# Performance work log

Hardware: AMD Instinct MI355X
Metric: run time of the kernel (lower is better)

The kernel has to match this reference:

```python
import jax, jax.numpy as jnp
import numpy as np

N, E = 50000, 800000
F_IN, F_OUT, H = 128, 16, 8
NEG_SLOPE = 0.2  # PyG GATConv default
EPS = 1e-5       # LayerNorm eps


def setup_inputs() -> dict:
    key = jax.random.key(0)
    ks = jax.random.split(key, 8)
    x = jax.random.normal(ks[0], (N, F_IN), dtype=jnp.float32)
    edge_index = jax.random.randint(ks[1], (2, E), 0, N, dtype=jnp.int32)
    s_in = 1.0 / np.sqrt(F_IN)
    s_f = 1.0 / np.sqrt(F_OUT)
    W = jax.random.normal(ks[2], (F_IN, H * F_OUT), dtype=jnp.float32) * s_in
    att_src = jax.random.normal(ks[3], (H, F_OUT), dtype=jnp.float32) * s_f
    att_dst = jax.random.normal(ks[4], (H, F_OUT), dtype=jnp.float32) * s_f
    bias = jnp.zeros((H * F_OUT,), dtype=jnp.float32)
    gamma = jnp.ones((H * F_OUT,), dtype=jnp.float32)
    beta = jnp.zeros((H * F_OUT,), dtype=jnp.float32)
    return {"x": x, "edge_index": edge_index, "W": W, "att_src": att_src,
            "att_dst": att_dst, "bias": bias, "gamma": gamma, "beta": beta}


def _gat_layer(x, edge_index, W, att_src, att_dst, bias, gamma, beta):
    n = x.shape[0]
    # add self loops (PyG GATConv default add_self_loops=True)
    loop = jnp.arange(n, dtype=edge_index.dtype)
    src = jnp.concatenate([edge_index[0], loop])  # message source j
    dst = jnp.concatenate([edge_index[1], loop])  # message target i

    xp = (x @ W).reshape(n, H, F_OUT)                      # [N,H,F]
    a_src = jnp.einsum('nhf,hf->nh', xp, att_src)          # [N,H]
    a_dst = jnp.einsum('nhf,hf->nh', xp, att_dst)          # [N,H]

    e = a_src[src] + a_dst[dst]                            # [E+N,H]
    e = jax.nn.leaky_relu(e, NEG_SLOPE)
    # softmax over incoming edges per destination node
    m = jax.ops.segment_max(e, dst, num_segments=n)        # [N,H]
    e = jnp.exp(e - m[dst])
    z = jax.ops.segment_sum(e, dst, num_segments=n)        # [N,H]
    alpha = e / jnp.where(z[dst] > 0, z[dst], 1.0)         # [E+N,H]

    msg = alpha[:, :, None] * xp[src]                      # [E+N,H,F]
    out = jax.ops.segment_sum(msg, dst, num_segments=n)    # [N,H,F]
    out = out.reshape(n, H * F_OUT) + bias

    # LayerNorm over feature dim
    mu = out.mean(axis=-1, keepdims=True)
    var = out.var(axis=-1, keepdims=True)
    return (out - mu) * jax.lax.rsqrt(var + EPS) * gamma + beta


def reference(x, edge_index, W, att_src, att_dst, bias, gamma, beta):
    return _gat_layer(x, edge_index, W, att_src, att_dst, bias, gamma, beta)
```

## Files before the change

kernel.cpp:

```cpp
#include <hip/hip_runtime.h>
#include <math.h>

#define F_IN 128
#define NHD 8
#define FEAT 128
#define NEG_SLOPE 0.2f
#define LN_EPS 1e-5f
#define BSH 7
#define BMSK 127
#define NPQ 16
#define CAP 48
#define EPB 2048
#define NBMAX 512
#define BCAP 6144
#define WCOLS 144

typedef __bf16 v8bf __attribute__((ext_vector_type(8)));
typedef __bf16 v2bf __attribute__((ext_vector_type(2)));
typedef float f32x4 __attribute__((ext_vector_type(4)));

__global__ __launch_bounds__(256) void k_wt(const float* __restrict__ W,
                                            const float* __restrict__ att_src,
                                            const float* __restrict__ att_dst,
                                            __bf16* __restrict__ WT,
                                            int* __restrict__ gcnt, int NB) {
    int idx = blockIdx.x * 256 + threadIdx.x;
    if (idx < NB) gcnt[idx] = 0;
    int c = idx >> 7, k = idx & 127;
    float v;
    if (c < 128) {
        v = W[k * 128 + c];
    } else if (c < 136) {
        int h = c - 128;
        float s = 0.f;
#pragma unroll
        for (int f = 0; f < 16; ++f) s += W[k * 128 + h * 16 + f] * att_src[h * 16 + f];
        v = s;
    } else {
        int h = c - 136;
        float s = 0.f;
#pragma unroll
        for (int f = 0; f < 16; ++f) s += W[k * 128 + h * 16 + f] * att_dst[h * 16 + f];
        v = s;
    }
    WT[c * 128 + k] = (__bf16)v;
}

__global__ __launch_bounds__(512) void k_fused(const float* __restrict__ x,
                                               const __bf16* __restrict__ WT,
                                               __bf16* __restrict__ xp16,
                                               float* __restrict__ a_src,
                                               float* __restrict__ a_dst,
                                               const int* __restrict__ src,
                                               const int* __restrict__ dst,
                                               unsigned int* __restrict__ sorted2,
                                               int* __restrict__ gcnt,
                                               int n, int E, int Ga) {
    __shared__ __align__(16) char smem[34816];
    if ((int)blockIdx.x < Ga) {
        unsigned int* sorted_l = (unsigned int*)smem;
        int* lcnt = (int*)(smem + 8192);
        int* loff = (int*)(smem + 8192 + 2048);
        int* wtot = (int*)(smem + 8192 + 2048 + 2052);
        int* wexcl = (int*)(smem + 8192 + 2048 + 2052 + 32);
        int* goff = (int*)(smem + 8192 + 2048 + 2052 + 64);
        int NB = (n + BMSK) >> BSH;
        int tid = threadIdx.x, lane = tid & 63, wid = tid >> 6;
        long base0 = (long)blockIdx.x * EPB;
        long total = (long)E + n;
        if (tid < NB) lcnt[tid] = 0;
        __syncthreads();

        int s0[4], d0[4];
        bool val[4];
        long e0 = base0 + (long)tid * 4;
        if (e0 + 3 < E) {
            int4 sv = *(const int4*)(src + e0);
            int4 dv = *(const int4*)(dst + e0);
            s0[0] = sv.x; s0[1] = sv.y; s0[2] = sv.z; s0[3] = sv.w;
            d0[0] = dv.x; d0[1] = dv.y; d0[2] = dv.z; d0[3] = dv.w;
            val[0] = val[1] = val[2] = val[3] = true;
        } else {
#pragma unroll
            for (int j = 0; j < 4; ++j) {
                long e = e0 + j;
                val[j] = (e < total);
                s0[j] = d0[j] = 0;
                if (val[j]) {
                    if (e < E) { s0[j] = src[e]; d0[j] = dst[e]; }
                    else { s0[j] = d0[j] = (int)(e - E); }
                }
            }
        }
#pragma unroll
        for (int j = 0; j < 4; ++j)
            if (val[j]) atomicAdd(&lcnt[d0[j] >> BSH], 1);
        __syncthreads();

        int v = (tid < NB) ? lcnt[tid] : 0;
        int xx = v;
#pragma unroll
        for (int o = 1; o < 64; o <<= 1) {
            int t2 = __shfl_up(xx, o);
            if (lane >= o) xx += t2;
        }
        if (lane == 63) wtot[wid] = xx;
        __syncthreads();
        if (wid == 0 && lane < 8) {
            int s = wtot[lane];
            int y = s;
#pragma unroll
            for (int o = 1; o < 8; o <<= 1) {
                int t2 = __shfl_up(y, o);
                if (lane >= o) y += t2;
            }
            wexcl[lane] = y - s;
        }
        __syncthreads();
        int excl = wexcl[wid] + xx - v;
        if (tid < NB) loff[tid] = excl;
        if (tid == NB - 1) loff[NB] = excl + v;
        __syncthreads();
        if (tid < NB) lcnt[tid] = loff[tid];
        __syncthreads();
#pragma unroll
        for (int j = 0; j < 4; ++j) {
            if (val[j]) {
                int b = d0[j] >> BSH;
                int pos = atomicAdd(&lcnt[b], 1);
                sorted_l[pos] = ((unsigned)b << 23) | ((unsigned)s0[j] << 7) |
                                (unsigned)(d0[j] & BMSK);
            }
        }
        __syncthreads();
        if (tid < NB) {
            int len = loff[tid + 1] - loff[tid];
            goff[tid] = (len > 0) ? atomicAdd(&gcnt[tid], len) : 0;
        }
        __syncthreads();
        int tv = loff[NB];
        for (int i = tid; i < tv; i += 512) {
            unsigned int u = sorted_l[i];
            int b = (int)(u >> 23);
            int r = goff[b] + (i - loff[b]);
            if (r < BCAP)
                sorted2[(long)b * BCAP + r] = u & 0x7FFFFFu;
        }
    } else {
        __bf16 (*xs)[136] = (__bf16 (*)[136])smem;
        __bf16 (*ot)[136] = (__bf16 (*)[136])(smem + 17408);
        int gb = blockIdx.x - Ga;
        int tid = threadIdx.x;
        int rowbase = gb * 64;
        {
            int i4 = tid;
#pragma unroll
            for (int rep = 0; rep < 4; ++rep, i4 += 512) {
                int r = i4 >> 5, c4 = i4 & 31;
                int gr = rowbase + r; if (gr > n - 1) gr = n - 1;
                float4 xv = *(const float4*)(x + (long)gr * 128 + c4 * 4);
                __bf16* p = &xs[r][c4 * 4];
                p[0] = (__bf16)xv.x; p[1] = (__bf16)xv.y;
                p[2] = (__bf16)xv.z; p[3] = (__bf16)xv.w;
            }
        }
        __syncthreads();
        int wv = tid >> 6;
        int lane = tid & 63;
        int m = lane & 15, quad = lane >> 4;
        int colbase = wv * 16;
        const __bf16* wcol = WT + (colbase + m) * 128;
        v8bf wf[4];
#pragma unroll
        for (int kk = 0; kk < 4; ++kk)
            wf[kk] = *(const v8bf*)(wcol + kk * 32 + quad * 8);
        v8bf wf2[4];
        if (wv < 4) {
            const __bf16* wcol2 = WT + (128 + m) * 128;
#pragma unroll
            for (int kk = 0; kk < 4; ++kk)
                wf2[kk] = *(const v8bf*)(wcol2 + kk * 32 + quad * 8);
        }
#pragma unroll
        for (int t = 0; t < 4; ++t) {
            int rb = t * 16;
            f32x4 acc = {0.f, 0.f, 0.f, 0.f};
#pragma unroll
            for (int kk = 0; kk < 4; ++kk) {
                v8bf a = *(const v8bf*)(&xs[rb + m][kk * 32 + quad * 8]);
                acc = __builtin_amdgcn_mfma_f32_16x16x32_bf16(a, wf[kk], acc, 0, 0, 0);
            }
#pragma unroll
            for (int r = 0; r < 4; ++r)
                ot[rb + quad * 4 + r][colbase + m] = (__bf16)acc[r];
        }
        if (wv < 4) {
            int rb = wv * 16;
            f32x4 acc = {0.f, 0.f, 0.f, 0.f};
#pragma unroll
            for (int kk = 0; kk < 4; ++kk) {
                v8bf a = *(const v8bf*)(&xs[rb + m][kk * 32 + quad * 8]);
                acc = __builtin_amdgcn_mfma_f32_16x16x32_bf16(a, wf2[kk], acc, 0, 0, 0);
            }
#pragma unroll
            for (int r = 0; r < 4; ++r) {
                int row = rowbase + rb + quad * 4 + r;
                if (row < n) {
                    if (m < 8) a_src[row * 8 + m] = acc[r];
                    else       a_dst[row * 8 + (m - 8)] = acc[r];
                }
            }
        }
        __syncthreads();
        int r0 = tid >> 4, c8 = tid & 15;
#pragma unroll
        for (int pass = 0; pass < 2; ++pass) {
            int r = r0 + pass * 32;
            int gr = rowbase + r;
            if (gr < n) {
                v8bf vv = *(const v8bf*)(&ot[r][c8 * 8]);
                *(v8bf*)(xp16 + (long)gr * FEAT + c8 * 8) = vv;
            }
        }
    }
}

__global__ __launch_bounds__(256) void k_ba(const unsigned int* __restrict__ sorted2,
                                            const int* __restrict__ bcnt,
                                            const float* __restrict__ a_src,
                                            const float* __restrict__ a_dst,
                                            const __bf16* __restrict__ xp16,
                                            const float* __restrict__ bias,
                                            const float* __restrict__ gamma,
                                            const float* __restrict__ beta,
                                            const int* __restrict__ src,
                                            const int* __restrict__ dst,
                                            float* __restrict__ out, int n, int E) {
    __shared__ int slds[NPQ * CAP];
    __shared__ int lc[NPQ];
    __shared__ float adst_s[NPQ * NHD];
    int b = blockIdx.x >> 3;
    int q = blockIdx.x & 7;
    int tid = threadIdx.x;
    int node0 = (b << BSH) + q * NPQ;
    if (tid < NPQ) lc[tid] = 0;
    if (tid < NPQ * NHD) {
        int nd = node0 + (tid >> 3);
        adst_s[tid] = (nd < n) ? a_dst[nd * NHD + (tid & 7)] : 0.f;
    }
    __syncthreads();

    int cnt_b = bcnt[b]; if (cnt_b > BCAP) cnt_b = BCAP;
    const unsigned int* sg = sorted2 + (long)b * BCAP;
    int qlo = q * NPQ;
    for (int i = tid; i < cnt_b; i += 256) {
        unsigned int u = sg[i];
        int dl = (int)(u & BMSK) - qlo;
        if ((unsigned)dl < (unsigned)NPQ) {
            int p = atomicAdd(&lc[dl], 1);
            if (p < CAP) slds[dl * CAP + p] = (int)(u >> BSH);
        }
    }
    __syncthreads();
    if (tid < NPQ) {
        int cc = lc[tid]; if (cc > CAP) cc = CAP;
        int pad = (cc + 7) & ~7; if (pad > CAP) pad = CAP;
        for (int p = cc; p < pad; ++p) slds[tid * CAP + p] = 0;
    }
    __syncthreads();

    int lane = tid & 63, wv = tid >> 6;
    int h = lane & 7, j8 = lane >> 3;
    float2 bs = *(const float2*)(bias + 2 * lane);
    float2 g  = *(const float2*)(gamma + 2 * lane);
    float2 bt = *(const float2*)(beta + 2 * lane);

    for (int i = wv; i < NPQ; i += 4) {
        int node = node0 + i;
        if (node >= n) break;
        int cnt = lc[i];
        float acc0 = 0.f, acc1 = 0.f, inv;

        if (cnt <= CAP) {
            const int* row = slds + i * CAP;
            float b_h = adst_s[i * NHD + h];
            float zacc = 0.f;
            for (int base = 0; base < cnt; base += 8) {
                int s_my = row[base + j8];
                float e = a_src[s_my * NHD + h] + b_h;
                e = e > 0.f ? e : NEG_SLOPE * e;
                float w_my = (base + j8 < cnt) ? __expf(e) : 0.f;
                zacc += w_my;
                int ss[8];
#pragma unroll
                for (int j = 0; j < 8; ++j) ss[j] = row[base + j];
                float2 vals[8];
#pragma unroll
                for (int j = 0; j < 8; ++j) {
                    v2bf p = *(const v2bf*)(xp16 + (long)ss[j] * FEAT + 2 * lane);
                    vals[j] = make_float2((float)p[0], (float)p[1]);
                }
#pragma unroll
                for (int j = 0; j < 8; ++j) {
                    float w = __shfl(w_my, j * 8 + j8);
                    acc0 = fmaf(w, vals[j].x, acc0);
                    acc1 = fmaf(w, vals[j].y, acc1);
                }
            }
            zacc += __shfl_xor(zacc, 8);
            zacc += __shfl_xor(zacc, 16);
            zacc += __shfl_xor(zacc, 32);
            float z = __shfl(zacc, j8);
            inv = 1.f / z;
        } else {
            float b_h = a_dst[node * NHD + j8];
            float z = 0.f;
            {
                float e = a_src[node * NHD + j8] + b_h;
                e = e > 0.f ? e : NEG_SLOPE * e;
                float w = __expf(e);
                z += w;
                v2bf p = *(const v2bf*)(xp16 + (long)node * FEAT + 2 * lane);
                acc0 = fmaf(w, (float)p[0], acc0);
                acc1 = fmaf(w, (float)p[1], acc1);
            }
            for (int base = 0; base < E; base += 64) {
                int e = base + lane;
                int sv = 0;
                bool mt = false;
                if (e < E) { mt = (dst[e] == node); if (mt) sv = src[e]; }
                unsigned long long mask = __ballot(mt);
                while (mask) {
                    int bl = __ffsll(mask) - 1;
                    mask &= mask - 1;
                    int s = __shfl(sv, bl);
                    float ee = a_src[s * NHD + j8] + b_h;
                    ee = ee > 0.f ? ee : NEG_SLOPE * ee;
                    float w = __expf(ee);
                    z += w;
                    v2bf p = *(const v2bf*)(xp16 + (long)s * FEAT + 2 * lane);
                    acc0 = fmaf(w, (float)p[0], acc0);
                    acc1 = fmaf(w, (float)p[1], acc1);
                }
            }
            inv = 1.f / z;
        }

        float v0 = acc0 * inv + bs.x;
        float v1 = acc1 * inv + bs.y;
        float ssum = v0 + v1;
        float ssq = v0 * v0 + v1 * v1;
#pragma unroll
        for (int o = 32; o > 0; o >>= 1) {
            ssum += __shfl_xor(ssum, o);
            ssq += __shfl_xor(ssq, o);
        }
        float mu = ssum * (1.0f / FEAT);
        float var = ssq * (1.0f / FEAT) - mu * mu;
        float rs = rsqrtf(var + LN_EPS);
        float2 o2;
        o2.x = (v0 - mu) * rs * g.x + bt.x;
        o2.y = (v1 - mu) * rs * g.y + bt.y;
        *(float2*)(out + (long)node * FEAT + 2 * lane) = o2;
    }
}

extern "C" void kernel_launch(void* const* d_in, const int* in_sizes, int n_in,
                              void* d_out, int out_size, void* d_ws, size_t ws_size,
                              hipStream_t stream) {
    const float* x = (const float*)d_in[0];
    const int* edge_index = (const int*)d_in[1];
    const float* W = (const float*)d_in[2];
    const float* att_src = (const float*)d_in[3];
    const float* att_dst = (const float*)d_in[4];
    const float* bias = (const float*)d_in[5];
    const float* gamma = (const float*)d_in[6];
    const float* beta = (const float*)d_in[7];
    float* out = (float*)d_out;

    int n = in_sizes[0] / F_IN;
    int E = in_sizes[1] / 2;
    const int* src = edge_index;
    const int* dst = edge_index + E;
    int NB = (n + BMSK) >> BSH;
    int Ga = (E + n + EPB - 1) / EPB;
    int Gg = (n + 63) / 64;

    char* ws = (char*)d_ws;
    __bf16* WT   = (__bf16*)ws;                    ws += (size_t)WCOLS * 128 * 2;
    __bf16* xp16 = (__bf16*)ws;                    ws += (size_t)n * FEAT * 2;
    float* a_src = (float*)ws;                     ws += (size_t)n * NHD * 4;
    float* a_dst = (float*)ws;                     ws += (size_t)n * NHD * 4;
    unsigned int* sorted2 = (unsigned int*)ws;     ws += (size_t)NB * BCAP * 4;
    int* gcnt = (int*)ws;                          ws += (size_t)NB * 4;

    k_wt<<<72, 256, 0, stream>>>(W, att_src, att_dst, WT, gcnt, NB);
    k_fused<<<Ga + Gg, 512, 0, stream>>>(x, WT, xp16, a_src, a_dst,
                                         src, dst, sorted2, gcnt, n, E, Ga);
    k_ba<<<NB * 8, 256, 0, stream>>>(sorted2, gcnt, a_src, a_dst, xp16,
                                     bias, gamma, beta, src, dst, out, n, E);
}
```

Before: 153.1 us.

## Process two nodes per wave in aggregation and double edges per bucketing block

```diff
diff --git a/kernel.cpp b/kernel.cpp
--- a/kernel.cpp
+++ b/kernel.cpp
@@ -8,9 +8,9 @@
 #define LN_EPS 1e-5f
 #define BSH 7
 #define BMSK 127
-#define NPQ 16
+#define NPQ 32
 #define CAP 48
-#define EPB 2048
+#define EPB 4096
 #define NBMAX 512
 #define BCAP 6144
 #define WCOLS 144
@@ -59,11 +59,11 @@
     __shared__ __align__(16) char smem[34816];
     if ((int)blockIdx.x < Ga) {
         unsigned int* sorted_l = (unsigned int*)smem;
-        int* lcnt = (int*)(smem + 8192);
-        int* loff = (int*)(smem + 8192 + 2048);
-        int* wtot = (int*)(smem + 8192 + 2048 + 2052);
-        int* wexcl = (int*)(smem + 8192 + 2048 + 2052 + 32);
-        int* goff = (int*)(smem + 8192 + 2048 + 2052 + 64);
+        int* lcnt = (int*)(smem + 16384);
+        int* loff = (int*)(smem + 16384 + 2048);
+        int* wtot = (int*)(smem + 16384 + 2048 + 2052);
+        int* wexcl = (int*)(smem + 16384 + 2048 + 2052 + 32);
+        int* goff = (int*)(smem + 16384 + 2048 + 2052 + 64);
         int NB = (n + BMSK) >> BSH;
         int tid = threadIdx.x, lane = tid & 63, wid = tid >> 6;
         long base0 = (long)blockIdx.x * EPB;
@@ -71,18 +71,23 @@
         if (tid < NB) lcnt[tid] = 0;
         __syncthreads();
 
-        int s0[4], d0[4];
-        bool val[4];
-        long e0 = base0 + (long)tid * 4;
-        if (e0 + 3 < E) {
-            int4 sv = *(const int4*)(src + e0);
-            int4 dv = *(const int4*)(dst + e0);
-            s0[0] = sv.x; s0[1] = sv.y; s0[2] = sv.z; s0[3] = sv.w;
-            d0[0] = dv.x; d0[1] = dv.y; d0[2] = dv.z; d0[3] = dv.w;
-            val[0] = val[1] = val[2] = val[3] = true;
+        int s0[8], d0[8];
+        bool val[8];
+        long e0 = base0 + (long)tid * 8;
+        if (e0 + 7 < E) {
+            int4 sa = *(const int4*)(src + e0);
+            int4 sb = *(const int4*)(src + e0 + 4);
+            int4 da = *(const int4*)(dst + e0);
+            int4 db = *(const int4*)(dst + e0 + 4);
+            s0[0] = sa.x; s0[1] = sa.y; s0[2] = sa.z; s0[3] = sa.w;
+            s0[4] = sb.x; s0[5] = sb.y; s0[6] = sb.z; s0[7] = sb.w;
+            d0[0] = da.x; d0[1] = da.y; d0[2] = da.z; d0[3] = da.w;
+            d0[4] = db.x; d0[5] = db.y; d0[6] = db.z; d0[7] = db.w;
+#pragma unroll
+            for (int j = 0; j < 8; ++j) val[j] = true;
         } else {
 #pragma unroll
-            for (int j = 0; j < 4; ++j) {
+            for (int j = 0; j < 8; ++j) {
                 long e = e0 + j;
                 val[j] = (e < total);
                 s0[j] = d0[j] = 0;
@@ -93,7 +98,7 @@
             }
         }
 #pragma unroll
-        for (int j = 0; j < 4; ++j)
+        for (int j = 0; j < 8; ++j)
             if (val[j]) atomicAdd(&lcnt[d0[j] >> BSH], 1);
         __syncthreads();
 
@@ -124,7 +129,7 @@
         if (tid < NB) lcnt[tid] = loff[tid];
         __syncthreads();
 #pragma unroll
-        for (int j = 0; j < 4; ++j) {
+        for (int j = 0; j < 8; ++j) {
             if (val[j]) {
                 int b = d0[j] >> BSH;
                 int pos = atomicAdd(&lcnt[b], 1);
@@ -223,6 +228,104 @@
             }
         }
     }
+}
+
+__device__ __forceinline__ float lrelu(float e) {
+    return e > 0.f ? e : NEG_SLOPE * e;
+}
+
+__device__ __forceinline__ void agg_lds(const int* __restrict__ row, int cnt,
+                                        float b_h,
+                                        const float* __restrict__ a_src,
+                                        const __bf16* __restrict__ xp16,
+                                        int lane, int h, int j8,
+                                        float& acc0, float& acc1, float& z) {
+    float zacc = 0.f;
+    for (int base = 0; base < cnt; base += 8) {
+        int s_my = row[base + j8];
+        float e = lrelu(a_src[s_my * NHD + h] + b_h);
+        float w_my = (base + j8 < cnt) ? __expf(e) : 0.f;
+        zacc += w_my;
+        int ss[8];
+#pragma unroll
+        for (int j = 0; j < 8; ++j) ss[j] = row[base + j];
+        float2 vals[8];
+#pragma unroll
+        for (int j = 0; j < 8; ++j) {
+            v2bf p = *(const v2bf*)(xp16 + (long)ss[j] * FEAT + 2 * lane);
+            vals[j] = make_float2((float)p[0], (float)p[1]);
+        }
+#pragma unroll
+        for (int j = 0; j < 8; ++j) {
+            float w = __shfl(w_my, j * 8 + j8);
+            acc0 = fmaf(w, vals[j].x, acc0);
+            acc1 = fmaf(w, vals[j].y, acc1);
+        }
+    }
+    zacc += __shfl_xor(zacc, 8);
+    zacc += __shfl_xor(zacc, 16);
+    zacc += __shfl_xor(zacc, 32);
+    z = __shfl(zacc, j8);
+}
+
+__device__ __forceinline__ void agg_fallback(int node,
+                                             const float* __restrict__ a_src,
+                                             const float* __restrict__ a_dst,
+                                             const __bf16* __restrict__ xp16,
+                                             const int* __restrict__ src,
+                                             const int* __restrict__ dst,
+                                             int E, int lane, int j8,
+                                             float& acc0, float& acc1, float& z) {
+    float b_h = a_dst[node * NHD + j8];
+    z = 0.f;
+    {
+        float e = lrelu(a_src[node * NHD + j8] + b_h);
+        float w = __expf(e);
+        z += w;
+        v2bf p = *(const v2bf*)(xp16 + (long)node * FEAT + 2 * lane);
+        acc0 = fmaf(w, (float)p[0], acc0);
+        acc1 = fmaf(w, (float)p[1], acc1);
+    }
+    for (int base = 0; base < E; base += 64) {
+        int e = base + lane;
+        int sv = 0;
+        bool mt = false;
+        if (e < E) { mt = (dst[e] == node); if (mt) sv = src[e]; }
+        unsigned long long mask = __ballot(mt);
+        while (mask) {
+            int bl = __ffsll(mask) - 1;
+            mask &= mask - 1;
+            int s = __shfl(sv, bl);
+            float ee = lrelu(a_src[s * NHD + j8] + b_h);
+            float w = __expf(ee);
+            z += w;
+            v2bf p = *(const v2bf*)(xp16 + (long)s * FEAT + 2 * lane);
+            acc0 = fmaf(w, (float)p[0], acc0);
+            acc1 = fmaf(w, (float)p[1], acc1);
+        }
+    }
+}
+
+__device__ __forceinline__ void ln_store(float acc0, float acc1, float inv,
+                                         float2 bs, float2 g, float2 bt,
+                                         float* __restrict__ out, int node,
+                                         int lane) {
+    float v0 = acc0 * inv + bs.x;
+    float v1 = acc1 * inv + bs.y;
+    float ssum = v0 + v1;
+    float ssq = v0 * v0 + v1 * v1;
+#pragma unroll
+    for (int o = 32; o > 0; o >>= 1) {
+        ssum += __shfl_xor(ssum, o);
+        ssq += __shfl_xor(ssq, o);
+    }
+    float mu = ssum * (1.0f / FEAT);
+    float var = ssq * (1.0f / FEAT) - mu * mu;
+    float rs = rsqrtf(var + LN_EPS);
+    float2 o2;
+    o2.x = (v0 - mu) * rs * g.x + bt.x;
+    o2.y = (v1 - mu) * rs * g.y + bt.y;
+    *(float2*)(out + (long)node * FEAT + 2 * lane) = o2;
 }
 
 __global__ __launch_bounds__(256) void k_ba(const unsigned int* __restrict__ sorted2,
@@ -239,12 +342,12 @@
     __shared__ int slds[NPQ * CAP];
     __shared__ int lc[NPQ];
     __shared__ float adst_s[NPQ * NHD];
-    int b = blockIdx.x >> 3;
-    int q = blockIdx.x & 7;
+    int b = blockIdx.x >> 2;
+    int q = blockIdx.x & 3;
     int tid = threadIdx.x;
     int node0 = (b << BSH) + q * NPQ;
     if (tid < NPQ) lc[tid] = 0;
-    if (tid < NPQ * NHD) {
+    {
         int nd = node0 + (tid >> 3);
         adst_s[tid] = (nd < n) ? a_dst[nd * NHD + (tid & 7)] : 0.f;
     }
@@ -275,93 +378,105 @@
     float2 g  = *(const float2*)(gamma + 2 * lane);
     float2 bt = *(const float2*)(beta + 2 * lane);
 
-    for (int i = wv; i < NPQ; i += 4) {
-        int node = node0 + i;
-        if (node >= n) break;
-        int cnt = lc[i];
-        float acc0 = 0.f, acc1 = 0.f, inv;
-
-        if (cnt <= CAP) {
-            const int* row = slds + i * CAP;
-            float b_h = adst_s[i * NHD + h];
-            float zacc = 0.f;
-            for (int base = 0; base < cnt; base += 8) {
-                int s_my = row[base + j8];
-                float e = a_src[s_my * NHD + h] + b_h;
-                e = e > 0.f ? e : NEG_SLOPE * e;
-                float w_my = (base + j8 < cnt) ? __expf(e) : 0.f;
-                zacc += w_my;
-                int ss[8];
-#pragma unroll
-                for (int j = 0; j < 8; ++j) ss[j] = row[base + j];
-                float2 vals[8];
-#pragma unroll
-                for (int j = 0; j < 8; ++j) {
-                    v2bf p = *(const v2bf*)(xp16 + (long)ss[j] * FEAT + 2 * lane);
-                    vals[j] = make_float2((float)p[0], (float)p[1]);
-                }
-#pragma unroll
-                for (int j = 0; j < 8; ++j) {
-                    float w = __shfl(w_my, j * 8 + j8);
-                    acc0 = fmaf(w, vals[j].x, acc0);
-                    acc1 = fmaf(w, vals[j].y, acc1);
-                }
-            }
-            zacc += __shfl_xor(zacc, 8);
-            zacc += __shfl_xor(zacc, 16);
-            zacc += __shfl_xor(zacc, 32);
-            float z = __shfl(zacc, j8);
-            inv = 1.f / z;
+    for (int t = 0; t < 4; ++t) {
+        int iA = wv * 8 + 2 * t;
+        int iB = iA + 1;
+        int nodeA = node0 + iA;
+        int nodeB = node0 + iB;
+        if (nodeA >= n) break;
+        bool haveB = (nodeB < n);
+        int cntA = lc[iA];
+        int cntB = haveB ? lc[iB] : 0;
+        float aA0 = 0.f, aA1 = 0.f, aB0 = 0.f, aB1 = 0.f;
+        float zA = 0.f, zB = 0.f;
+
+        if (cntA <= CAP && cntB <= CAP) {
+            const int* rowA = slds + iA * CAP;
+            const int* rowB = slds + iB * CAP;
+            float bhA = adst_s[iA * NHD + h];
+            float bhB = haveB ? adst_s[iB * NHD + h] : 0.f;
+            float zaccA = 0.f, zaccB = 0.f;
+            int mx = cntA > cntB ? cntA : cntB;
+            for (int base = 0; base < mx; base += 8) {
+                bool qa = base < cntA, qb = base < cntB;
+                int ssA[8], ssB[8];
+                float2 vA[8], vB[8];
+                if (qa) {
+#pragma unroll
+                    for (int j = 0; j < 8; ++j) ssA[j] = rowA[base + j];
+#pragma unroll
+                    for (int j = 0; j < 8; ++j) {
+                        v2bf p = *(const v2bf*)(xp16 + (long)ssA[j] * FEAT + 2 * lane);
+                        vA[j] = make_float2((float)p[0], (float)p[1]);
+                    }
+                }
+                if (qb) {
+#pragma unroll
+                    for (int j = 0; j < 8; ++j) ssB[j] = rowB[base + j];
+#pragma unroll
+                    for (int j = 0; j < 8; ++j) {
+                        v2bf p = *(const v2bf*)(xp16 + (long)ssB[j] * FEAT + 2 * lane);
+                        vB[j] = make_float2((float)p[0], (float)p[1]);
+                    }
+                }
+                float wA = 0.f, wB = 0.f;
+                if (qa) {
+                    int s = rowA[base + j8];
+                    float e = lrelu(a_src[s * NHD + h] + bhA);
+                    wA = (base + j8 < cntA) ? __expf(e) : 0.f;
+                    zaccA += wA;
+                }
+                if (qb) {
+                    int s = rowB[base + j8];
+                    float e = lrelu(a_src[s * NHD + h] + bhB);
+                    wB = (base + j8 < cntB) ? __expf(e) : 0.f;
+                    zaccB += wB;
+                }
+                if (qa) {
+#pragma unroll
+                    for (int j = 0; j < 8; ++j) {
+                        float w = __shfl(wA, j * 8 + j8);
+                        aA0 = fmaf(w, vA[j].x, aA0);
+                        aA1 = fmaf(w, vA[j].y, aA1);
+                    }
+                }
+                if (qb) {
+#pragma unroll
+                    for (int j = 0; j < 8; ++j) {
+                        float w = __shfl(wB, j * 8 + j8);
+                        aB0 = fmaf(w, vB[j].x, aB0);
+                        aB1 = fmaf(w, vB[j].y, aB1);
+                    }
+                }
+            }
+            zaccA += __shfl_xor(zaccA, 8);
+            zaccA += __shfl_xor(zaccA, 16);
+            zaccA += __shfl_xor(zaccA, 32);
+            zA = __shfl(zaccA, j8);
+            zaccB += __shfl_xor(zaccB, 8);
+            zaccB += __shfl_xor(zaccB, 16);
+            zaccB += __shfl_xor(zaccB, 32);
+            zB = __shfl(zaccB, j8);
         } else {
-            float b_h = a_dst[node * NHD + j8];
-            float z = 0.f;
-            {
-                float e = a_src[node * NHD + j8] + b_h;
-                e = e > 0.f ? e : NEG_SLOPE * e;
-                float w = __expf(e);
-                z += w;
-                v2bf p = *(const v2bf*)(xp16 + (long)node * FEAT + 2 * lane);
-                acc0 = fmaf(w, (float)p[0], acc0);
-                acc1 = fmaf(w, (float)p[1], acc1);
-            }
-            for (int base = 0; base < E; base += 64) {
-                int e = base + lane;
-                int sv = 0;
-                bool mt = false;
-                if (e < E) { mt = (dst[e] == node); if (mt) sv = src[e]; }
-                unsigned long long mask = __ballot(mt);
-                while (mask) {
-                    int bl = __ffsll(mask) - 1;
-                    mask &= mask - 1;
-                    int s = __shfl(sv, bl);
-                    float ee = a_src[s * NHD + j8] + b_h;
-                    ee = ee > 0.f ? ee : NEG_SLOPE * ee;
-                    float w = __expf(ee);
-                    z += w;
-                    v2bf p = *(const v2bf*)(xp16 + (long)s * FEAT + 2 * lane);
-                    acc0 = fmaf(w, (float)p[0], acc0);
-                    acc1 = fmaf(w, (float)p[1], acc1);
-                }
-            }
-            inv = 1.f / z;
-        }
-
-        float v0 = acc0 * inv + bs.x;
-        float v1 = acc1 * inv + bs.y;
-        float ssum = v0 + v1;
-        float ssq = v0 * v0 + v1 * v1;
-#pragma unroll
-        for (int o = 32; o > 0; o >>= 1) {
-            ssum += __shfl_xor(ssum, o);
-            ssq += __shfl_xor(ssq, o);
-        }
-        float mu = ssum * (1.0f / FEAT);
-        float var = ssq * (1.0f / FEAT) - mu * mu;
-        float rs = rsqrtf(var + LN_EPS);
-        float2 o2;
-        o2.x = (v0 - mu) * rs * g.x + bt.x;
-        o2.y = (v1 - mu) * rs * g.y + bt.y;
-        *(float2*)(out + (long)node * FEAT + 2 * lane) = o2;
+            if (cntA <= CAP)
+                agg_lds(slds + iA * CAP, cntA, adst_s[iA * NHD + h],
+                        a_src, xp16, lane, h, j8, aA0, aA1, zA);
+            else
+                agg_fallback(nodeA, a_src, a_dst, xp16, src, dst, E,
+                             lane, j8, aA0, aA1, zA);
+            if (haveB) {
+                if (cntB <= CAP)
+                    agg_lds(slds + iB * CAP, cntB, adst_s[iB * NHD + h],
+                            a_src, xp16, lane, h, j8, aB0, aB1, zB);
+                else
+                    agg_fallback(nodeB, a_src, a_dst, xp16, src, dst, E,
+                                 lane, j8, aB0, aB1, zB);
+            }
+        }
+
+        ln_store(aA0, aA1, 1.f / zA, bs, g, bt, out, nodeA, lane);
+        if (haveB)
+            ln_store(aB0, aB1, 1.f / zB, bs, g, bt, out, nodeB, lane);
     }
 }
 
@@ -397,6 +512,6 @@
     k_wt<<<72, 256, 0, stream>>>(W, att_src, att_dst, WT, gcnt, NB);
     k_fused<<<Ga + Gg, 512, 0, stream>>>(x, WT, xp16, a_src, a_dst,
                                          src, dst, sorted2, gcnt, n, E, Ga);
-    k_ba<<<NB * 8, 256, 0, stream>>>(sorted2, gcnt, a_src, a_dst, xp16,
+    k_ba<<<NB * 4, 256, 0, stream>>>(sorted2, gcnt, a_src, a_dst, xp16,
                                      bias, gamma, beta, src, dst, out, n, E);
 }
```

Result: slower. 168.6 us (+10.1%).
